# Performance work log

Hardware: AMD Instinct MI355X
Metric: run time of the kernel (lower is better)

The kernel has to match this reference:

```python
import jax, jax.numpy as jnp
import numpy as np

B, S, E, NH = 1, 2048, 1024, 8
DH = E // NH
EPS_BACKEND = 1e-6  # eps in parallel_stabilized_simple
EPS_NORM = 1e-5     # MultiHeadLayerNorm (group_norm) eps


def setup_inputs() -> dict:
    key = jax.random.key(0)
    ks = jax.random.split(key, 8)
    q = jax.random.normal(ks[0], (B, S, E), jnp.float32)
    k = jax.random.normal(ks[1], (B, S, E), jnp.float32)
    v = jax.random.normal(ks[2], (B, S, E), jnp.float32)
    # gate Linear params: weight (NH, 3E), bias (NH). Small scale so gates are
    # in a realistic regime (fgate bias ~ linspace(3,6) per the torch init).
    igate_w = jax.random.normal(ks[3], (NH, 3 * E), jnp.float32) * 0.02
    igate_b = jax.random.normal(ks[4], (NH,), jnp.float32) * 0.1
    fgate_w = jax.random.normal(ks[5], (NH, 3 * E), jnp.float32) * 0.02
    fgate_b = jnp.linspace(3.0, 6.0, NH).astype(jnp.float32)
    norm_w = 1.0 + 0.1 * jax.random.normal(ks[6], (E,), jnp.float32)
    return dict(q=q, k=k, v=v, igate_w=igate_w, igate_b=igate_b,
                fgate_w=fgate_w, fgate_b=fgate_b, norm_w=norm_w)


def reference(q, k, v, igate_w, igate_b, fgate_w, fgate_b, norm_w):
    Bq, Sq, Eq = q.shape
    nh = igate_w.shape[0]
    dh = Eq // nh
    # gate pre-activations from concatenated q,k,v
    gate_in = jnp.concatenate([q, k, v], axis=-1)             # (B,S,3E)
    ig = jnp.transpose(gate_in @ igate_w.T + igate_b, (0, 2, 1))  # (B,NH,S)
    fg = jnp.transpose(gate_in @ fgate_w.T + fgate_b, (0, 2, 1))  # (B,NH,S)
    # split heads: (B,NH,S,DH)
    qh = q.reshape(Bq, Sq, nh, dh).transpose(0, 2, 1, 3)
    kh = k.reshape(Bq, Sq, nh, dh).transpose(0, 2, 1, 3)
    vh = v.reshape(Bq, Sq, nh, dh).transpose(0, 2, 1, 3)
    # cumulative log forget gates; decay matrix entry (t,s) = cs[t]-cs[s]
    log_f_cum = jnp.cumsum(jax.nn.log_sigmoid(fg), axis=-1)   # (B,NH,S)
    log_fg_mat = log_f_cum[:, :, :, None] - log_f_cum[:, :, None, :]  # (B,NH,S,S)
    ltr = jnp.tril(jnp.ones((Sq, Sq), dtype=bool))            # causal mask
    log_D = jnp.where(ltr, log_fg_mat + ig[:, :, None, :], -jnp.inf)
    # row-wise stabilizer
    max_log_D = jnp.max(log_D, axis=-1, keepdims=True)        # (B,NH,S,1)
    D = jnp.exp(log_D - max_log_D)
    qk = jnp.einsum('bhsd,bhtd->bhst', qh, kh) / jnp.sqrt(jnp.float32(dh))
    C = qk * D
    normalizer = jnp.maximum(jnp.abs(jnp.sum(C, axis=-1, keepdims=True)),
                             jnp.exp(-max_log_D))
    h = jnp.einsum('bhst,bhtd->bhsd', C / (normalizer + EPS_BACKEND), vh)
    # MultiHeadLayerNorm == group_norm with NH groups over (NH*DH), per-channel weight
    mean = jnp.mean(h, axis=-1, keepdims=True)
    var = jnp.var(h, axis=-1, keepdims=True)
    h_norm = (h - mean) / jnp.sqrt(var + EPS_NORM)
    h_norm = h_norm * norm_w.reshape(nh, dh)[None, :, None, :]
    return h_norm.transpose(0, 2, 1, 3).reshape(Bq, Sq, Eq)
```

## Files before the change

kernel.cpp:

```cpp
#include <hip/hip_runtime.h>
#include <hip/hip_bf16.h>
#include <math.h>

#define S_LEN 2048
#define E_DIM 1024
#define NHEAD 8
#define DH 128
#define E3 3072

typedef short bf16x8 __attribute__((ext_vector_type(8)));
typedef short bf16x4 __attribute__((ext_vector_type(4)));
typedef float f32x4 __attribute__((ext_vector_type(4)));
typedef float f32x16 __attribute__((ext_vector_type(16)));

#define MFMA3216(a,b,c) __builtin_amdgcn_mfma_f32_32x32x16_bf16(a,b,c,0,0,0)
#define Z16 {0.f,0.f,0.f,0.f,0.f,0.f,0.f,0.f,0.f,0.f,0.f,0.f,0.f,0.f,0.f,0.f}
#define CROW(r) (((r)&3) + 8*((r)>>2))

__device__ __forceinline__ unsigned short f2bf(float f){
  union{float f; unsigned u;} x; x.f = f;
  unsigned r = x.u + 0x7FFF + ((x.u>>16)&1);
  return (unsigned short)(r>>16);
}

__device__ __forceinline__ unsigned cvtpk(float lo, float hi){
  unsigned r;
  asm("v_cvt_pk_bf16_f32 %0, %1, %2" : "=v"(r) : "v"(lo), "v"(hi));
  return r;
}

__device__ __forceinline__ float logsigf(float x){
  return fminf(x, 0.f) - log1pf(expf(-fabsf(x)));
}

typedef const __attribute__((address_space(1))) unsigned int* gas1_t;
typedef __attribute__((address_space(3))) unsigned int* las3_t;
__device__ __forceinline__ void stage16(const ushort* g, ushort* l){
  __builtin_amdgcn_global_load_lds((gas1_t)(const void*)g, (las3_t)(void*)l, 16, 0, 0);
}

__global__ __launch_bounds__(256) void gates_qk(
    const float* __restrict__ q, const float* __restrict__ k, const float* __restrict__ v,
    const float* __restrict__ igw, const float* __restrict__ igb,
    const float* __restrict__ fgw, const float* __restrict__ fgb,
    float* __restrict__ ig_out, float* __restrict__ lsf_out,
    ushort* __restrict__ qbo, ushort* __restrict__ kbo){
  const int t0 = blockIdx.x*4;
  const int tid = threadIdx.x;
  const int lane = tid & 63, wv = tid >> 6;
  float acc[64];
  #pragma unroll
  for (int a=0;a<64;++a) acc[a]=0.f;
  const float sc = 0.08838834764831845f;
  #pragma unroll
  for (int step=0; step<3; ++step){
    const float* src = (step==0)? q : ((step==1)? k : v);
    float4 in4[4];
    #pragma unroll
    for (int r=0;r<4;++r) in4[r] = ((const float4*)src)[(size_t)(t0+r)*256 + tid];
    if (step==0){
      #pragma unroll
      for (int r=0;r<4;++r){
        ushort4 o; o.x=f2bf(in4[r].x*sc); o.y=f2bf(in4[r].y*sc);
        o.z=f2bf(in4[r].z*sc); o.w=f2bf(in4[r].w*sc);
        ((ushort4*)qbo)[(size_t)(t0+r)*256 + tid] = o;
      }
    } else if (step==1){
      #pragma unroll
      for (int r=0;r<4;++r){
        ushort4 o; o.x=f2bf(in4[r].x); o.y=f2bf(in4[r].y);
        o.z=f2bf(in4[r].z); o.w=f2bf(in4[r].w);
        ((ushort4*)kbo)[(size_t)(t0+r)*256 + tid] = o;
      }
    }
    const int wj = step*256 + tid;
    #pragma unroll
    for (int o=0;o<8;++o){
      float4 wI = ((const float4*)igw)[o*768 + wj];
      float4 wF = ((const float4*)fgw)[o*768 + wj];
      #pragma unroll
      for (int r=0;r<4;++r){
        acc[o*4+r]    = fmaf(in4[r].x, wI.x, acc[o*4+r]);
        acc[o*4+r]    = fmaf(in4[r].y, wI.y, acc[o*4+r]);
        acc[o*4+r]    = fmaf(in4[r].z, wI.z, acc[o*4+r]);
        acc[o*4+r]    = fmaf(in4[r].w, wI.w, acc[o*4+r]);
        acc[32+o*4+r] = fmaf(in4[r].x, wF.x, acc[32+o*4+r]);
        acc[32+o*4+r] = fmaf(in4[r].y, wF.y, acc[32+o*4+r]);
        acc[32+o*4+r] = fmaf(in4[r].z, wF.z, acc[32+o*4+r]);
        acc[32+o*4+r] = fmaf(in4[r].w, wF.w, acc[32+o*4+r]);
      }
    }
  }
  int cnt = 32;
  #pragma unroll
  for (int s=0; s<6; ++s){
    const bool hib = (lane >> s) & 1;
    #pragma unroll
    for (int a=0; a<32; ++a){
      if (a < cnt){
        float sent = hib ? acc[a] : acc[a+cnt];
        float got = __shfl_xor(sent, 1<<s, 64);
        acc[a] = (hib ? acc[a+cnt] : acc[a]) + got;
      }
    }
    cnt >>= 1;
  }
  __shared__ float red[4][64];
  red[wv][lane] = acc[0];
  __syncthreads();
  if (tid < 64){
    float tot = red[0][tid]+red[1][tid]+red[2][tid]+red[3][tid];
    int a = (int)(__brev((unsigned)tid) >> 26);
    int f = a >> 5, o = (a>>2)&7, r = a&3;
    int t = t0 + r;
    if (f==0) ig_out[o*S_LEN + t] = tot + igb[o];
    else      lsf_out[o*S_LEN + t] = logsigf(tot + fgb[o]);
  }
}

__global__ __launch_bounds__(256) void scan_kernel(
    const float* __restrict__ ig, const float* __restrict__ lsf,
    float* __restrict__ cs_out, float* __restrict__ M_out, float* __restrict__ m_out){
  const int h = blockIdx.x;
  const int tid = threadIdx.x;
  __shared__ float tt[256];
  const int base = tid*8;
  const float* src = lsf + h*S_LEN;
  float loc[8]; float tot = 0.f;
  #pragma unroll
  for (int i=0;i<8;++i){ tot += src[base+i]; loc[i]=tot; }
  tt[tid]=tot; __syncthreads();
  for (int off=1; off<256; off<<=1){
    float add = (tid>=off)? tt[tid-off] : 0.f;
    __syncthreads();
    tt[tid] += add;
    __syncthreads();
  }
  const float excl = tt[tid] - tot;
  float csv[8];
  #pragma unroll
  for (int i=0;i<8;++i){ csv[i] = excl + loc[i]; cs_out[h*S_LEN+base+i]=csv[i]; }
  const float* igp = ig + h*S_LEN;
  float mloc[8], mval[8]; float mtot = -INFINITY;
  #pragma unroll
  for (int i=0;i<8;++i){
    float m = igp[base+i] - csv[i];
    mval[i] = m;
    mtot = fmaxf(mtot, m);
    mloc[i] = mtot;
  }
  __syncthreads();
  tt[tid]=mtot; __syncthreads();
  for (int off=1; off<256; off<<=1){
    float add = (tid>=off)? tt[tid-off] : -INFINITY;
    __syncthreads();
    tt[tid] = fmaxf(tt[tid], add);
    __syncthreads();
  }
  const float exclm = (tid>0)? tt[tid-1] : -INFINITY;
  #pragma unroll
  for (int i=0;i<8;++i){
    M_out[h*S_LEN+base+i] = fmaxf(exclm, mloc[i]);
    m_out[h*S_LEN+base+i] = mval[i];
  }
}

__global__ __launch_bounds__(256) void vtrans(
    const float* __restrict__ v, ushort* __restrict__ vt){
  const int s0 = blockIdx.x*64, d0 = blockIdx.y*64, h = blockIdx.z;
  __shared__ float T[64][65];
  const int r = threadIdx.x>>2, cq = threadIdx.x&3;
  #pragma unroll
  for (int i=0;i<4;++i){
    int col = cq*16 + i*4;
    float4 val = *(const float4*)(v + (size_t)(s0+r)*E_DIM + h*DH + d0 + col);
    T[r][col]=val.x; T[r][col+1]=val.y; T[r][col+2]=val.z; T[r][col+3]=val.w;
  }
  __syncthreads();
  ushort tmp[16];
  #pragma unroll
  for (int i=0;i<16;++i) tmp[i] = f2bf(T[cq*16+i][r]);
  ushort* dst = vt + ((size_t)(h*DH + d0 + r))*S_LEN + s0 + cq*16;
  uint4 o0, o1;
  ushort* p0 = (ushort*)&o0; ushort* p1 = (ushort*)&o1;
  #pragma unroll
  for (int i=0;i<8;++i){ p0[i]=tmp[i]; p1[i]=tmp[8+i]; }
  *(uint4*)dst = o0;
  *(uint4*)(dst+8) = o1;
}

__global__ __launch_bounds__(256, 2) void mlstm_mfma6(
    const ushort* __restrict__ qb, const ushort* __restrict__ kb,
    const ushort* __restrict__ vt,
    const float* __restrict__ csb, const float* __restrict__ Mxb,
    const float* __restrict__ mbb,
    const float* __restrict__ nw, float* __restrict__ out){
  const int h = blockIdx.x;
  const int qt = 63 - blockIdx.y;
  const int tid = threadIdx.x, l = tid & 63;
  const int sq = tid >> 6;
  const int l31 = l & 31, l15 = l & 15, hi = l >> 5;

  __shared__ __align__(16) float UNI[4*32*132];
  __shared__ float MB[128];
  __shared__ float rsL[4][32];
  ushort* Kb = (ushort*)UNI;
  ushort* Vb = Kb + 16384;
  float*  Part = UNI;

  const int hS = h*S_LEN;
  const ushort* kbh = kb + h*DH;
  const ushort* vth = vt + (size_t)h*DH*S_LEN;
  const float*  mh  = mbb + hS;
  const int t0 = qt*32;
  const int NT = (t0 + 31)/128 + 1;
  const int tgq = t0 + l31;
  const float Mq = Mxb[hS + tgq];

  bf16x8 qf0,qf1,qf2,qf3,qf4,qf5,qf6,qf7;
  { const ushort* qs = qb + (size_t)tgq*E_DIM + h*DH + hi*8;
    qf0 = *(const bf16x8*)(qs+0);   qf1 = *(const bf16x8*)(qs+16);
    qf2 = *(const bf16x8*)(qs+32);  qf3 = *(const bf16x8*)(qs+48);
    qf4 = *(const bf16x8*)(qs+64);  qf5 = *(const bf16x8*)(qs+80);
    qf6 = *(const bf16x8*)(qs+96);  qf7 = *(const bf16x8*)(qs+112); }

  f32x16 a0 = Z16, a1 = Z16, a2 = Z16, a3 = Z16;
  float rsq = 0.f;

#define STAGE6(ktv) {                                                        \
    _Pragma("unroll")                                                        \
    for (int i_=0;i_<8;++i_){                                                \
      const int L_ = tid + i_*256; const int row_ = L_>>4, pc_ = L_&15;      \
      stage16(kbh + (size_t)((ktv)*128+row_)*E_DIM + ((pc_^(row_&15))<<3),   \
              Kb + (size_t)L_*8); }                                          \
    _Pragma("unroll")                                                        \
    for (int i_=0;i_<8;++i_){                                                \
      const int L_ = tid + i_*256; const int d_ = L_>>4, pc_ = L_&15;        \
      stage16(vth + (size_t)d_*S_LEN + (ktv)*128 + ((pc_^(d_&15))<<3),       \
              Vb + (size_t)L_*8); }                                          \
    if (tid < 32)                                                            \
      stage16((const ushort*)(mh + (ktv)*128) + tid*8,                       \
              (ushort*)MB + tid*8); }

#define LV6(dt, cs) (*(const bf16x8*)(Vb + (size_t)((dt)*32+l31)*128 + (((cs)^l15)<<3)))

  for (int kt=0; kt<NT; ++kt){
    if (kt) __syncthreads();
    STAGE6(kt);
    __syncthreads();

    const ushort* kbase = Kb + (size_t)(sq*32 + l31)*128;
    f32x16 cc = Z16;
    { bf16x8 ka;
      ka = *(const bf16x8*)(kbase + (((0*2+hi)^l15)<<3)); cc = MFMA3216(ka, qf0, cc);
      ka = *(const bf16x8*)(kbase + (((1*2+hi)^l15)<<3)); cc = MFMA3216(ka, qf1, cc);
      ka = *(const bf16x8*)(kbase + (((2*2+hi)^l15)<<3)); cc = MFMA3216(ka, qf2, cc);
      ka = *(const bf16x8*)(kbase + (((3*2+hi)^l15)<<3)); cc = MFMA3216(ka, qf3, cc);
      ka = *(const bf16x8*)(kbase + (((4*2+hi)^l15)<<3)); cc = MFMA3216(ka, qf4, cc);
      ka = *(const bf16x8*)(kbase + (((5*2+hi)^l15)<<3)); cc = MFMA3216(ka, qf5, cc);
      ka = *(const bf16x8*)(kbase + (((6*2+hi)^l15)<<3)); cc = MFMA3216(ka, qf6, cc);
      ka = *(const bf16x8*)(kbase + (((7*2+hi)^l15)<<3)); cc = MFMA3216(ka, qf7, cc); }

    bf16x8 fE, fO;
    {
      const int sb_ = kt*128 + sq*32 + 4*hi;
      const f32x4 mA_ = *(const f32x4*)&MB[sq*32 +  0 + 4*hi];
      const f32x4 mB_ = *(const f32x4*)&MB[sq*32 +  8 + 4*hi];
      const f32x4 mC_ = *(const f32x4*)&MB[sq*32 + 16 + 4*hi];
      const f32x4 mD_ = *(const f32x4*)&MB[sq*32 + 24 + 4*hi];
      float p0  = (sb_+0  <= tgq) ? cc[0] *__expf(mA_[0]-Mq) : 0.f;
      float p1  = (sb_+1  <= tgq) ? cc[1] *__expf(mA_[1]-Mq) : 0.f;
      float p2  = (sb_+2  <= tgq) ? cc[2] *__expf(mA_[2]-Mq) : 0.f;
      float p3  = (sb_+3  <= tgq) ? cc[3] *__expf(mA_[3]-Mq) : 0.f;
      float p4  = (sb_+8  <= tgq) ? cc[4] *__expf(mB_[0]-Mq) : 0.f;
      float p5  = (sb_+9  <= tgq) ? cc[5] *__expf(mB_[1]-Mq) : 0.f;
      float p6  = (sb_+10 <= tgq) ? cc[6] *__expf(mB_[2]-Mq) : 0.f;
      float p7  = (sb_+11 <= tgq) ? cc[7] *__expf(mB_[3]-Mq) : 0.f;
      float p8  = (sb_+16 <= tgq) ? cc[8] *__expf(mC_[0]-Mq) : 0.f;
      float p9  = (sb_+17 <= tgq) ? cc[9] *__expf(mC_[1]-Mq) : 0.f;
      float p10 = (sb_+18 <= tgq) ? cc[10]*__expf(mC_[2]-Mq) : 0.f;
      float p11 = (sb_+19 <= tgq) ? cc[11]*__expf(mC_[3]-Mq) : 0.f;
      float p12 = (sb_+24 <= tgq) ? cc[12]*__expf(mD_[0]-Mq) : 0.f;
      float p13 = (sb_+25 <= tgq) ? cc[13]*__expf(mD_[1]-Mq) : 0.f;
      float p14 = (sb_+26 <= tgq) ? cc[14]*__expf(mD_[2]-Mq) : 0.f;
      float p15 = (sb_+27 <= tgq) ? cc[15]*__expf(mD_[3]-Mq) : 0.f;
      rsq += ((p0+p1)+(p2+p3))+((p4+p5)+(p6+p7))
           + ((p8+p9)+(p10+p11))+((p12+p13)+(p14+p15));
      unsigned A0_=cvtpk(p0,p1),  A1_=cvtpk(p2,p3);
      unsigned B0_=cvtpk(p4,p5),  B1_=cvtpk(p6,p7);
      unsigned C0_=cvtpk(p8,p9),  C1_=cvtpk(p10,p11);
      unsigned D0_=cvtpk(p12,p13),D1_=cvtpk(p14,p15);
      unsigned A0x_=(unsigned)__shfl_xor((int)A0_,32,64);
      unsigned B0x_=(unsigned)__shfl_xor((int)B0_,32,64);
      unsigned A1x_=(unsigned)__shfl_xor((int)A1_,32,64);
      unsigned B1x_=(unsigned)__shfl_xor((int)B1_,32,64);
      unsigned C0x_=(unsigned)__shfl_xor((int)C0_,32,64);
      unsigned D0x_=(unsigned)__shfl_xor((int)D0_,32,64);
      unsigned C1x_=(unsigned)__shfl_xor((int)C1_,32,64);
      unsigned D1x_=(unsigned)__shfl_xor((int)D1_,32,64);
      { unsigned* u_ = (unsigned*)&fE;
        u_[0] = hi ? B0x_ : A0_;  u_[1] = hi ? B1x_ : A1_;
        u_[2] = hi ? B0_  : A0x_; u_[3] = hi ? B1_  : A1x_; }
      { unsigned* u_ = (unsigned*)&fO;
        u_[0] = hi ? D0x_ : C0_;  u_[1] = hi ? D1x_ : C1_;
        u_[2] = hi ? D0_  : C0x_; u_[3] = hi ? D1_  : C1x_; }
    }

    a0 = MFMA3216(fE, LV6(0, sq*4 + 0 + hi), a0);
    a1 = MFMA3216(fE, LV6(1, sq*4 + 0 + hi), a1);
    a2 = MFMA3216(fE, LV6(2, sq*4 + 0 + hi), a2);
    a3 = MFMA3216(fE, LV6(3, sq*4 + 0 + hi), a3);
    a0 = MFMA3216(fO, LV6(0, sq*4 + 2 + hi), a0);
    a1 = MFMA3216(fO, LV6(1, sq*4 + 2 + hi), a1);
    a2 = MFMA3216(fO, LV6(2, sq*4 + 2 + hi), a2);
    a3 = MFMA3216(fO, LV6(3, sq*4 + 2 + hi), a3);
  }

  __syncthreads();
  #pragma unroll
  for (int r=0;r<16;++r){
    const int qrow = CROW(r) + 4*hi;
    float* pr = Part + (size_t)(sq*32 + qrow)*132 + l31;
    pr[0]  = a0[r];
    pr[32] = a1[r];
    pr[64] = a2[r];
    pr[96] = a3[r];
  }
  rsq += __shfl_xor(rsq, 32, 64);
  if (l < 32) rsL[sq][l31] = rsq;
  __syncthreads();

  {
    const int q = tid >> 3, dg = tid & 7;
    f32x4 os0={0.f,0.f,0.f,0.f}, os1=os0, os2=os0, os3=os0;
    #pragma unroll
    for (int w2=0; w2<4; ++w2){
      const float* pb = Part + (size_t)(w2*32 + q)*132 + dg*16;
      os0 += *(const f32x4*)(pb+0);
      os1 += *(const f32x4*)(pb+4);
      os2 += *(const f32x4*)(pb+8);
      os3 += *(const f32x4*)(pb+12);
    }
    const float rstot = rsL[0][q]+rsL[1][q]+rsL[2][q]+rsL[3][q];
    const int tq = t0 + q;
    const float en = __expf(-(csb[hS+tq] + Mxb[hS+tq]));
    const float iv = 1.f/(fmaxf(fabsf(rstot), en) + 1e-6f);
    f32x4 h0, h1, h2, h3;
    h0[0]=os0[0]*iv; h0[1]=os0[1]*iv; h0[2]=os0[2]*iv; h0[3]=os0[3]*iv;
    h1[0]=os1[0]*iv; h1[1]=os1[1]*iv; h1[2]=os1[2]*iv; h1[3]=os1[3]*iv;
    h2[0]=os2[0]*iv; h2[1]=os2[1]*iv; h2[2]=os2[2]*iv; h2[3]=os2[3]*iv;
    h3[0]=os3[0]*iv; h3[1]=os3[1]*iv; h3[2]=os3[2]*iv; h3[3]=os3[3]*iv;
    float s1 = (h0[0]+h0[1]+h0[2]+h0[3]) + (h1[0]+h1[1]+h1[2]+h1[3])
             + (h2[0]+h2[1]+h2[2]+h2[3]) + (h3[0]+h3[1]+h3[2]+h3[3]);
    float s2 = (h0[0]*h0[0]+h0[1]*h0[1]+h0[2]*h0[2]+h0[3]*h0[3])
             + (h1[0]*h1[0]+h1[1]*h1[1]+h1[2]*h1[2]+h1[3]*h1[3])
             + (h2[0]*h2[0]+h2[1]*h2[1]+h2[2]*h2[2]+h2[3]*h2[3])
             + (h3[0]*h3[0]+h3[1]*h3[1]+h3[2]*h3[2]+h3[3]*h3[3]);
    s1 += __shfl_xor(s1, 1, 64);  s2 += __shfl_xor(s2, 1, 64);
    s1 += __shfl_xor(s1, 2, 64);  s2 += __shfl_xor(s2, 2, 64);
    s1 += __shfl_xor(s1, 4, 64);  s2 += __shfl_xor(s2, 4, 64);
    const float mean = s1*(1.f/128.f);
    const float var  = s2*(1.f/128.f) - mean*mean;
    const float rstd = rsqrtf(var + 1e-5f);
    const float* nb = nw + h*DH + dg*16;
    const f32x4 n0 = *(const f32x4*)(nb+0);
    const f32x4 n1 = *(const f32x4*)(nb+4);
    const f32x4 n2 = *(const f32x4*)(nb+8);
    const f32x4 n3 = *(const f32x4*)(nb+12);
    float* ob = out + (size_t)tq*E_DIM + h*DH + dg*16;
    f32x4 o0v, o1v, o2v, o3v;
    o0v[0]=(h0[0]-mean)*rstd*n0[0]; o0v[1]=(h0[1]-mean)*rstd*n0[1];
    o0v[2]=(h0[2]-mean)*rstd*n0[2]; o0v[3]=(h0[3]-mean)*rstd*n0[3];
    o1v[0]=(h1[0]-mean)*rstd*n1[0]; o1v[1]=(h1[1]-mean)*rstd*n1[1];
    o1v[2]=(h1[2]-mean)*rstd*n1[2]; o1v[3]=(h1[3]-mean)*rstd*n1[3];
    o2v[0]=(h2[0]-mean)*rstd*n2[0]; o2v[1]=(h2[1]-mean)*rstd*n2[1];
    o2v[2]=(h2[2]-mean)*rstd*n2[2]; o2v[3]=(h2[3]-mean)*rstd*n2[3];
    o3v[0]=(h3[0]-mean)*rstd*n3[0]; o3v[1]=(h3[1]-mean)*rstd*n3[1];
    o3v[2]=(h3[2]-mean)*rstd*n3[2]; o3v[3]=(h3[3]-mean)*rstd*n3[3];
    *(f32x4*)(ob+0)  = o0v;
    *(f32x4*)(ob+4)  = o1v;
    *(f32x4*)(ob+8)  = o2v;
    *(f32x4*)(ob+12) = o3v;
  }
}

extern "C" void kernel_launch(void* const* d_in, const int* in_sizes, int n_in,
                              void* d_out, int out_size, void* d_ws, size_t ws_size,
                              hipStream_t stream) {
  const float* q   = (const float*)d_in[0];
  const float* k   = (const float*)d_in[1];
  const float* v   = (const float*)d_in[2];
  const float* igw = (const float*)d_in[3];
  const float* igb = (const float*)d_in[4];
  const float* fgw = (const float*)d_in[5];
  const float* fgb = (const float*)d_in[6];
  const float* nw  = (const float*)d_in[7];
  float* outp = (float*)d_out;

  float* ws  = (float*)d_ws;
  float* ig  = ws;
  float* lsf = ws + 1*NHEAD*S_LEN;
  float* csb = ws + 2*NHEAD*S_LEN;
  float* Mb  = ws + 3*NHEAD*S_LEN;
  float* mbf = ws + 4*NHEAD*S_LEN;
  ushort* qbb = (ushort*)(ws + 5*NHEAD*S_LEN);
  ushort* kbb = qbb + (size_t)S_LEN*E_DIM;
  ushort* vtb = kbb + (size_t)S_LEN*E_DIM;

  gates_qk<<<512, 256, 0, stream>>>(q, k, v, igw, igb, fgw, fgb, ig, lsf, qbb, kbb);
  scan_kernel<<<NHEAD, 256, 0, stream>>>(ig, lsf, csb, Mb, mbf);
  vtrans<<<dim3(S_LEN/64, DH/64, NHEAD), 256, 0, stream>>>(v, vtb);
  mlstm_mfma6<<<dim3(NHEAD, 64), 256, 0, stream>>>(qbb, kbb, vtb, csb, Mb, mbf, nw, outp);
}
```

Baseline: 60.79 us.

## Fuse V transpose into gate kernel and restructure gate reduction per wave

Removes the separate vtrans kernel: the gates kernel now writes the bf16 transposed V directly while it already reads v for the gate dot products, so v is read once. The gate kernel is also rebuilt: each block handles 8 timesteps, each wave owns two heads, and the cross-wave shared-memory reduction becomes an in-wave shuffle tree. The payoff is one fewer launch and less global traffic. In exchange the grid halves to 256 blocks, the bf16 conversion stores fall to a single wave per step, and the V^T stores are 16-byte writes strided by S_LEN, which may coalesce poorly.

```diff
diff --git a/kernel.cpp b/kernel.cpp
--- a/kernel.cpp
+++ b/kernel.cpp
@@ -44,59 +44,84 @@
     const float* __restrict__ igw, const float* __restrict__ igb,
     const float* __restrict__ fgw, const float* __restrict__ fgb,
     float* __restrict__ ig_out, float* __restrict__ lsf_out,
-    ushort* __restrict__ qbo, ushort* __restrict__ kbo){
-  const int t0 = blockIdx.x*4;
+    ushort* __restrict__ qbo, ushort* __restrict__ kbo, ushort* __restrict__ vto){
+  const int t0 = blockIdx.x*8;
   const int tid = threadIdx.x;
-  const int lane = tid & 63, wv = tid >> 6;
-  float acc[64];
-  #pragma unroll
-  for (int a=0;a<64;++a) acc[a]=0.f;
+  const int lane = tid & 63, w = tid >> 6;
   const float sc = 0.08838834764831845f;
+
+  float acc[32];
+  #pragma unroll
+  for (int a=0;a<32;++a) acc[a]=0.f;
+
+  const float4* wI0 = (const float4*)igw + (size_t)(2*w)*768;
+  const float4* wI1 = (const float4*)igw + (size_t)(2*w+1)*768;
+  const float4* wF0 = (const float4*)fgw + (size_t)(2*w)*768;
+  const float4* wF1 = (const float4*)fgw + (size_t)(2*w+1)*768;
+
   #pragma unroll
   for (int step=0; step<3; ++step){
     const float* src = (step==0)? q : ((step==1)? k : v);
-    float4 in4[4];
     #pragma unroll
-    for (int r=0;r<4;++r) in4[r] = ((const float4*)src)[(size_t)(t0+r)*256 + tid];
-    if (step==0){
+    for (int i=0;i<4;++i){
+      const int col = i*64 + lane;
+      float4 in4[8];
       #pragma unroll
-      for (int r=0;r<4;++r){
-        ushort4 o; o.x=f2bf(in4[r].x*sc); o.y=f2bf(in4[r].y*sc);
-        o.z=f2bf(in4[r].z*sc); o.w=f2bf(in4[r].w*sc);
-        ((ushort4*)qbo)[(size_t)(t0+r)*256 + tid] = o;
+      for (int r=0;r<8;++r)
+        in4[r] = ((const float4*)src)[(size_t)(t0+r)*256 + col];
+
+      if (step==0 && w==0){
+        #pragma unroll
+        for (int r=0;r<8;++r){
+          ushort4 o; o.x=f2bf(in4[r].x*sc); o.y=f2bf(in4[r].y*sc);
+          o.z=f2bf(in4[r].z*sc); o.w=f2bf(in4[r].w*sc);
+          ((ushort4*)qbo)[(size_t)(t0+r)*256 + col] = o;
+        }
+      } else if (step==1 && w==1){
+        #pragma unroll
+        for (int r=0;r<8;++r){
+          ushort4 o; o.x=f2bf(in4[r].x); o.y=f2bf(in4[r].y);
+          o.z=f2bf(in4[r].z); o.w=f2bf(in4[r].w);
+          ((ushort4*)kbo)[(size_t)(t0+r)*256 + col] = o;
+        }
+      } else if (step==2 && w==2){
+        #pragma unroll
+        for (int c=0;c<4;++c){
+          ushort tmp[8];
+          tmp[0]=f2bf(c==0?in4[0].x:c==1?in4[0].y:c==2?in4[0].z:in4[0].w);
+          tmp[1]=f2bf(c==0?in4[1].x:c==1?in4[1].y:c==2?in4[1].z:in4[1].w);
+          tmp[2]=f2bf(c==0?in4[2].x:c==1?in4[2].y:c==2?in4[2].z:in4[2].w);
+          tmp[3]=f2bf(c==0?in4[3].x:c==1?in4[3].y:c==2?in4[3].z:in4[3].w);
+          tmp[4]=f2bf(c==0?in4[4].x:c==1?in4[4].y:c==2?in4[4].z:in4[4].w);
+          tmp[5]=f2bf(c==0?in4[5].x:c==1?in4[5].y:c==2?in4[5].z:in4[5].w);
+          tmp[6]=f2bf(c==0?in4[6].x:c==1?in4[6].y:c==2?in4[6].z:in4[6].w);
+          tmp[7]=f2bf(c==0?in4[7].x:c==1?in4[7].y:c==2?in4[7].z:in4[7].w);
+          uint4 ov; ushort* pp=(ushort*)&ov;
+          #pragma unroll
+          for (int z=0;z<8;++z) pp[z]=tmp[z];
+          *(uint4*)(vto + (size_t)(col*4+c)*S_LEN + t0) = ov;
+        }
       }
-    } else if (step==1){
+
+      const int jj = step*256 + col;
+      const float4 a0 = wI0[jj], a1 = wI1[jj], b0 = wF0[jj], b1 = wF1[jj];
       #pragma unroll
-      for (int r=0;r<4;++r){
-        ushort4 o; o.x=f2bf(in4[r].x); o.y=f2bf(in4[r].y);
-        o.z=f2bf(in4[r].z); o.w=f2bf(in4[r].w);
-        ((ushort4*)kbo)[(size_t)(t0+r)*256 + tid] = o;
+      for (int r=0;r<8;++r){
+        float x=in4[r].x, y=in4[r].y, z=in4[r].z, u=in4[r].w;
+        acc[r]    = fmaf(x,a0.x,fmaf(y,a0.y,fmaf(z,a0.z,fmaf(u,a0.w,acc[r]))));
+        acc[8+r]  = fmaf(x,a1.x,fmaf(y,a1.y,fmaf(z,a1.z,fmaf(u,a1.w,acc[8+r]))));
+        acc[16+r] = fmaf(x,b0.x,fmaf(y,b0.y,fmaf(z,b0.z,fmaf(u,b0.w,acc[16+r]))));
+        acc[24+r] = fmaf(x,b1.x,fmaf(y,b1.y,fmaf(z,b1.z,fmaf(u,b1.w,acc[24+r]))));
       }
     }
-    const int wj = step*256 + tid;
-    #pragma unroll
-    for (int o=0;o<8;++o){
-      float4 wI = ((const float4*)igw)[o*768 + wj];
-      float4 wF = ((const float4*)fgw)[o*768 + wj];
-      #pragma unroll
-      for (int r=0;r<4;++r){
-        acc[o*4+r]    = fmaf(in4[r].x, wI.x, acc[o*4+r]);
-        acc[o*4+r]    = fmaf(in4[r].y, wI.y, acc[o*4+r]);
-        acc[o*4+r]    = fmaf(in4[r].z, wI.z, acc[o*4+r]);
-        acc[o*4+r]    = fmaf(in4[r].w, wI.w, acc[o*4+r]);
-        acc[32+o*4+r] = fmaf(in4[r].x, wF.x, acc[32+o*4+r]);
-        acc[32+o*4+r] = fmaf(in4[r].y, wF.y, acc[32+o*4+r]);
-        acc[32+o*4+r] = fmaf(in4[r].z, wF.z, acc[32+o*4+r]);
-        acc[32+o*4+r] = fmaf(in4[r].w, wF.w, acc[32+o*4+r]);
-      }
-    }
-  }
-  int cnt = 32;
-  #pragma unroll
-  for (int s=0; s<6; ++s){
+  }
+
+  int cnt = 16;
+  #pragma unroll
+  for (int s=0; s<5; ++s){
     const bool hib = (lane >> s) & 1;
     #pragma unroll
-    for (int a=0; a<32; ++a){
+    for (int a=0; a<16; ++a){
       if (a < cnt){
         float sent = hib ? acc[a] : acc[a+cnt];
         float got = __shfl_xor(sent, 1<<s, 64);
@@ -105,16 +130,14 @@
     }
     cnt >>= 1;
   }
-  __shared__ float red[4][64];
-  red[wv][lane] = acc[0];
-  __syncthreads();
-  if (tid < 64){
-    float tot = red[0][tid]+red[1][tid]+red[2][tid]+red[3][tid];
-    int a = (int)(__brev((unsigned)tid) >> 26);
-    int f = a >> 5, o = (a>>2)&7, r = a&3;
-    int t = t0 + r;
-    if (f==0) ig_out[o*S_LEN + t] = tot + igb[o];
-    else      lsf_out[o*S_LEN + t] = logsigf(tot + fgb[o]);
+  acc[0] += __shfl_xor(acc[0], 32, 64);
+  if (lane < 32){
+    const int a = (int)(__brev((unsigned)lane) >> 27);
+    const int p = a >> 4, hh = (a>>3)&1, r = a&7;
+    const int o = 2*w + hh;
+    const int t = t0 + r;
+    if (p==0) ig_out[o*S_LEN + t] = acc[0] + igb[o];
+    else      lsf_out[o*S_LEN + t] = logsigf(acc[0] + fgb[o]);
   }
 }
 
@@ -163,30 +186,6 @@
     M_out[h*S_LEN+base+i] = fmaxf(exclm, mloc[i]);
     m_out[h*S_LEN+base+i] = mval[i];
   }
-}
-
-__global__ __launch_bounds__(256) void vtrans(
-    const float* __restrict__ v, ushort* __restrict__ vt){
-  const int s0 = blockIdx.x*64, d0 = blockIdx.y*64, h = blockIdx.z;
-  __shared__ float T[64][65];
-  const int r = threadIdx.x>>2, cq = threadIdx.x&3;
-  #pragma unroll
-  for (int i=0;i<4;++i){
-    int col = cq*16 + i*4;
-    float4 val = *(const float4*)(v + (size_t)(s0+r)*E_DIM + h*DH + d0 + col);
-    T[r][col]=val.x; T[r][col+1]=val.y; T[r][col+2]=val.z; T[r][col+3]=val.w;
-  }
-  __syncthreads();
-  ushort tmp[16];
-  #pragma unroll
-  for (int i=0;i<16;++i) tmp[i] = f2bf(T[cq*16+i][r]);
-  ushort* dst = vt + ((size_t)(h*DH + d0 + r))*S_LEN + s0 + cq*16;
-  uint4 o0, o1;
-  ushort* p0 = (ushort*)&o0; ushort* p1 = (ushort*)&o1;
-  #pragma unroll
-  for (int i=0;i<8;++i){ p0[i]=tmp[i]; p1[i]=tmp[8+i]; }
-  *(uint4*)dst = o0;
-  *(uint4*)(dst+8) = o1;
 }
 
 __global__ __launch_bounds__(256, 2) void mlstm_mfma6(
@@ -407,8 +406,8 @@
   ushort* kbb = qbb + (size_t)S_LEN*E_DIM;
   ushort* vtb = kbb + (size_t)S_LEN*E_DIM;
 
-  gates_qk<<<512, 256, 0, stream>>>(q, k, v, igw, igb, fgw, fgb, ig, lsf, qbb, kbb);
+  gates_qk<<<S_LEN/8, 256, 0, stream>>>(q, k, v, igw, igb, fgw, fgb,
+                                        ig, lsf, qbb, kbb, vtb);
   scan_kernel<<<NHEAD, 256, 0, stream>>>(ig, lsf, csb, Mb, mbf);
-  vtrans<<<dim3(S_LEN/64, DH/64, NHEAD), 256, 0, stream>>>(v, vtb);
   mlstm_mfma6<<<dim3(NHEAD, 64), 256, 0, stream>>>(qbb, kbb, vtb, csb, Mb, mbf, nw, outp);
 }
```

Result: slower. 75.63 us (+24.4%).
